# Optimization experiments

Measured on AMD Instinct MI355X. Metric: run time of the kernel, lower is better.

## Reference

```python
import jax, jax.numpy as jnp
import numpy as np

ALPHABET = 26

def _shift(position, S):
    if position == 0:
        return jnp.zeros(S, dtype=jnp.int32)
    elif position == 1:
        return jnp.arange(S, dtype=jnp.int32) % ALPHABET
    elif position == 2:
        return jnp.arange(S, dtype=jnp.int32) // 26 + 1 % 26  # faithful to torch precedence: +1
    elif position == 3:
        return jnp.arange(S, dtype=jnp.int32) // 676 + 1 % 26
    raise ValueError('Invalid rotor position')


def setup_inputs() -> dict:
    key = jax.random.key(0)
    k1, k2 = jax.random.split(key)
    B, S = 128, 8192
    signalInput = jax.random.normal(k1, (B, S, ALPHABET), dtype=jnp.float32)
    # xavier_normal_ on a 26x26 matrix: std = sqrt(2/(26+26))
    std = float(np.sqrt(2.0 / (ALPHABET + ALPHABET)))
    rotor = jax.random.normal(k2, (ALPHABET, ALPHABET), dtype=jnp.float32) * std
    return {"signalInput": signalInput, "rotor": rotor}


def reference(signalInput, rotor):
    position = 1
    B, S, _ = signalInput.shape
    # L2-normalize rotor rows (torch.norm(dim=1, keepdim=True))
    rn = rotor / jnp.linalg.norm(rotor, axis=1, keepdims=True)  # [26,26]
    shift = _shift(position, S)                                  # [S]
    # one_hot((i + shift[s]) % 26) @ rn  ==  gather rn rows
    idx = (jnp.arange(ALPHABET, dtype=jnp.int32)[None, :] + shift[:, None]) % ALPHABET  # [S,26]
    M = rn[idx]                                                  # [S,26,26]
    # per-token 1x26 @ 26x26 bmm, batch-independent rotation matrix
    out = jnp.einsum('bsi,sij->bsj', signalInput, M)             # [B,S,26]
    return jax.nn.softmax(out, axis=2)
```

## Files before the change

### kernel.cpp

```cpp
#include <hip/hip_runtime.h>
#include <math.h>

#define ALPHA 26
#define TPB 256
#define ROWF 26
#define WAVEF (64 * ROWF)

typedef __attribute__((ext_vector_type(8))) short short8;
typedef __attribute__((ext_vector_type(4))) float float4v;
typedef __attribute__((address_space(3))) float lds_f;
typedef const __attribute__((address_space(1))) float glb_f;

__device__ __forceinline__ unsigned short f2bf(float f) {
    unsigned u = __builtin_bit_cast(unsigned, f);
    u += 0x7FFFu + ((u >> 16) & 1u);
    return (unsigned short)(u >> 16);
}

__global__ void rotor_norm_kernel(const float* __restrict__ rotor,
                                  unsigned short* __restrict__ rnb) {
    int k = threadIdx.x;
    if (k < 32) {
        if (k < ALPHA) {
            float ss = 0.f;
            #pragma unroll
            for (int j = 0; j < ALPHA; ++j) {
                float v = rotor[k * ALPHA + j];
                ss += v * v;
            }
            float inv = 1.0f / sqrtf(ss);
            #pragma unroll
            for (int n = 0; n < 32; ++n)
                rnb[k * 32 + n] = (n < ALPHA) ? f2bf(rotor[k * ALPHA + n] * inv)
                                              : (unsigned short)0;
        } else {
            #pragma unroll
            for (int n = 0; n < 32; ++n) rnb[k * 32 + n] = 0;
        }
    }
}

__global__ __launch_bounds__(TPB, 6) void rotor_main(
        const float* __restrict__ x,
        const unsigned short* __restrict__ rnb,
        float* __restrict__ out) {
    __shared__ float stage[4 * WAVEF];

    const int tid  = threadIdx.x;
    const int lane = tid & 63;
    const int wave = tid >> 6;
    const int n15  = lane & 15;
    const int quad = lane >> 4;
    const int waveF = wave * WAVEF;

    short8 bfrag0, bfrag1;
    #pragma unroll
    for (int j = 0; j < 8; ++j) {
        int k = quad * 8 + j;
        bfrag0[j] = (short)rnb[k * 32 + n15];
        bfrag1[j] = (short)rnb[k * 32 + 16 + n15];
    }

    const long long blockF = (long long)blockIdx.x * (TPB * ALPHA);
    const float* gin  = x   + blockF;
    float*       gout = out + blockF;

    #pragma unroll
    for (int it = 0; it < 6; ++it) {
        __builtin_amdgcn_global_load_lds(
            (glb_f*)(gin + waveF + it * 256 + lane * 4),
            (lds_f*)&stage[waveF + it * 256],
            16, 0, 0);
    }
    {
        float2 d = *(const float2*)(gin + waveF + 1536 + lane * 2);
        *(float2*)&stage[waveF + 1536 + lane * 2] = d;
    }
    asm volatile("s_waitcnt vmcnt(0)" ::: "memory");

    const int tokBase = blockIdx.x * TPB + wave * 64;
    float4v accA[4], accB[4];
    #pragma unroll
    for (int m = 0; m < 4; ++m) {
        accA[m] = (float4v){0.f, 0.f, 0.f, 0.f};
        accB[m] = (float4v){0.f, 0.f, 0.f, 0.f};
    }

    #pragma unroll
    for (int m = 0; m < 4; ++m) {
        const int tok = tokBase + m * 16 + n15;
        const int r = (tok & 8191) % 26;
        const int rowOff = waveF + (m * 16 + n15) * ROWF;
        const int k0 = quad * 8;
        int idx0 = k0 - r; if (idx0 < 0) idx0 += 26;

        short8 af;
        #pragma unroll
        for (int j = 0; j < 8; ++j) {
            int idx = idx0 + j; if (idx >= 26) idx -= 26;
            float v = stage[rowOff + idx];
            v = (k0 + j < ALPHA) ? v : 0.f;
            af[j] = (short)f2bf(v);
        }
        accA[m] = __builtin_amdgcn_mfma_f32_16x16x32_bf16(af, bfrag0, accA[m], 0, 0, 0);
        accB[m] = __builtin_amdgcn_mfma_f32_16x16x32_bf16(af, bfrag1, accB[m], 0, 0, 0);
    }

    #pragma unroll
    for (int m = 0; m < 4; ++m) {
        #pragma unroll
        for (int rg = 0; rg < 4; ++rg) {
            const int base = waveF + (m * 16 + quad * 4 + rg) * ROWF;
            stage[base + n15] = accA[m][rg];
            if (n15 < ALPHA - 16)
                stage[base + 16 + n15] = accB[m][rg];
        }
    }
    asm volatile("s_waitcnt lgkmcnt(0)" ::: "memory");

    const float* myrow = &stage[waveF + lane * ROWF];
    float v[ALPHA];
    #pragma unroll
    for (int j = 0; j < ALPHA; ++j) v[j] = myrow[j];
    float mx = v[0];
    #pragma unroll
    for (int j = 1; j < ALPHA; ++j) mx = fmaxf(mx, v[j]);
    float sum = 0.f;
    #pragma unroll
    for (int j = 0; j < ALPHA; ++j) { v[j] = __expf(v[j] - mx); sum += v[j]; }
    float inv = 1.0f / sum;
    float* wrow = &stage[waveF + lane * ROWF];
    #pragma unroll
    for (int j = 0; j < ALPHA; ++j) wrow[j] = v[j] * inv;

    #pragma unroll
    for (int it = 0; it < 6; ++it) {
        float4 d = *(const float4*)&stage[waveF + it * 256 + lane * 4];
        *(float4*)(gout + waveF + it * 256 + lane * 4) = d;
    }
    {
        float2 d = *(const float2*)&stage[waveF + 1536 + lane * 2];
        *(float2*)(gout + waveF + 1536 + lane * 2) = d;
    }
}

extern "C" void kernel_launch(void* const* d_in, const int* in_sizes, int n_in,
                              void* d_out, int out_size, void* d_ws, size_t ws_size,
                              hipStream_t stream) {
    const float* x     = (const float*)d_in[0];
    const float* rotor = (const float*)d_in[1];
    float* out = (float*)d_out;
    unsigned short* rnb = (unsigned short*)d_ws;

    rotor_norm_kernel<<<1, 64, 0, stream>>>(rotor, rnb);

    const int tokens = out_size / ALPHA;
    const int blocks = tokens / TPB;
    rotor_main<<<blocks, TPB, 0, stream>>>(x, rnb, out);
}
```

Before: 193.6 us.

## Make rotor kernel persistent with double-buffered LDS prefetch of next tile

Turns the one-tile-per-block main kernel into a persistent grid-stride loop over at most 768 blocks. Each block double-buffers LDS and issues async global-to-LDS loads for the next tile while computing the current one, so load latency overlaps with MFMA, softmax and stores. The rotor matrix is also stored transposed so each B fragment is a single vector load, and the tail copy now goes through global_load_lds too. In exchange, LDS use per block doubles and launch bounds drop to 3 blocks per CU, which lowers occupancy. Correctness also depends on the hand-written vmcnt count matching the number of loads in flight.

```diff
diff --git a/kernel.cpp b/kernel.cpp
--- a/kernel.cpp
+++ b/kernel.cpp
@@ -5,6 +5,8 @@
 #define TPB 256
 #define ROWF 26
 #define WAVEF (64 * ROWF)
+#define BUFF (4 * WAVEF)
+#define NBLK 768
 
 typedef __attribute__((ext_vector_type(8))) short short8;
 typedef __attribute__((ext_vector_type(4))) float float4v;
@@ -18,33 +20,39 @@
 }
 
 __global__ void rotor_norm_kernel(const float* __restrict__ rotor,
-                                  unsigned short* __restrict__ rnb) {
-    int k = threadIdx.x;
-    if (k < 32) {
-        if (k < ALPHA) {
-            float ss = 0.f;
+                                  unsigned short* __restrict__ rnbT) {
+    __shared__ float inv[32];
+    const int t = threadIdx.x;
+    if (t < 32) {
+        float s = 0.f;
+        if (t < ALPHA) {
             #pragma unroll
             for (int j = 0; j < ALPHA; ++j) {
-                float v = rotor[k * ALPHA + j];
-                ss += v * v;
+                float v = rotor[t * ALPHA + j];
+                s += v * v;
             }
-            float inv = 1.0f / sqrtf(ss);
-            #pragma unroll
-            for (int n = 0; n < 32; ++n)
-                rnb[k * 32 + n] = (n < ALPHA) ? f2bf(rotor[k * ALPHA + n] * inv)
-                                              : (unsigned short)0;
+            inv[t] = 1.0f / sqrtf(s);
         } else {
-            #pragma unroll
-            for (int n = 0; n < 32; ++n) rnb[k * 32 + n] = 0;
+            inv[t] = 0.f;
         }
+    }
+    __syncthreads();
+    const int n  = t >> 1;
+    const int k0 = (t & 1) * 16;
+    #pragma unroll
+    for (int kk = 0; kk < 16; ++kk) {
+        const int k = k0 + kk;
+        float v = (k < ALPHA && n < ALPHA) ? rotor[k * ALPHA + n] * inv[k] : 0.f;
+        rnbT[n * 32 + k] = f2bf(v);
     }
 }
 
-__global__ __launch_bounds__(TPB, 6) void rotor_main(
+__global__ __launch_bounds__(TPB, 3) void rotor_main(
         const float* __restrict__ x,
-        const unsigned short* __restrict__ rnb,
-        float* __restrict__ out) {
-    __shared__ float stage[4 * WAVEF];
+        const unsigned short* __restrict__ rnbT,
+        float* __restrict__ out,
+        int ntiles) {
+    __shared__ float stage[2 * BUFF];
 
     const int tid  = threadIdx.x;
     const int lane = tid & 63;
@@ -53,94 +61,100 @@
     const int quad = lane >> 4;
     const int waveF = wave * WAVEF;
 
-    short8 bfrag0, bfrag1;
-    #pragma unroll
-    for (int j = 0; j < 8; ++j) {
-        int k = quad * 8 + j;
-        bfrag0[j] = (short)rnb[k * 32 + n15];
-        bfrag1[j] = (short)rnb[k * 32 + 16 + n15];
-    }
+    short8 bf0 = *(const short8*)(rnbT + n15 * 32 + quad * 8);
+    short8 bf1 = *(const short8*)(rnbT + (n15 + 16) * 32 + quad * 8);
 
-    const long long blockF = (long long)blockIdx.x * (TPB * ALPHA);
-    const float* gin  = x   + blockF;
-    float*       gout = out + blockF;
+    int tile = blockIdx.x;
+    if (tile >= ntiles) return;
+    const int stride = gridDim.x;
 
-    #pragma unroll
-    for (int it = 0; it < 6; ++it) {
-        __builtin_amdgcn_global_load_lds(
-            (glb_f*)(gin + waveF + it * 256 + lane * 4),
-            (lds_f*)&stage[waveF + it * 256],
-            16, 0, 0);
-    }
-    {
-        float2 d = *(const float2*)(gin + waveF + 1536 + lane * 2);
-        *(float2*)&stage[waveF + 1536 + lane * 2] = d;
-    }
-    asm volatile("s_waitcnt vmcnt(0)" ::: "memory");
+    auto prefetch = [&](int buf, int t) {
+        const float* gp = x + (long long)t * (TPB * ALPHA) + waveF;
+        lds_f* lp = (lds_f*)&stage[buf * BUFF + waveF];
+        #pragma unroll
+        for (int it = 0; it < 6; ++it)
+            __builtin_amdgcn_global_load_lds((glb_f*)(gp + it * 256 + lane * 4),
+                                             lp + it * 256, 16, 0, 0);
+        __builtin_amdgcn_global_load_lds((glb_f*)(gp + 1536 + lane), lp + 1536, 4, 0, 0);
+        __builtin_amdgcn_global_load_lds((glb_f*)(gp + 1600 + lane), lp + 1600, 4, 0, 0);
+    };
 
-    const int tokBase = blockIdx.x * TPB + wave * 64;
-    float4v accA[4], accB[4];
-    #pragma unroll
-    for (int m = 0; m < 4; ++m) {
-        accA[m] = (float4v){0.f, 0.f, 0.f, 0.f};
-        accB[m] = (float4v){0.f, 0.f, 0.f, 0.f};
-    }
+    prefetch(0, tile);
 
-    #pragma unroll
-    for (int m = 0; m < 4; ++m) {
-        const int tok = tokBase + m * 16 + n15;
-        const int r = (tok & 8191) % 26;
-        const int rowOff = waveF + (m * 16 + n15) * ROWF;
-        const int k0 = quad * 8;
-        int idx0 = k0 - r; if (idx0 < 0) idx0 += 26;
+    int i = 0;
+    for (; tile < ntiles; tile += stride, ++i) {
+        if (i == 0) asm volatile("s_waitcnt vmcnt(0)" ::: "memory");
+        else        asm volatile("s_waitcnt vmcnt(7)" ::: "memory");
 
-        short8 af;
+        const int cur = i & 1;
+        const int tnext = tile + stride;
+        if (tnext < ntiles) prefetch(cur ^ 1, tnext);
+        asm volatile("" ::: "memory");
+
+        const int sbase   = cur * BUFF + waveF;
+        const int tokBase = tile * TPB + wave * 64;
+
+        float4v accA[4], accB[4];
         #pragma unroll
-        for (int j = 0; j < 8; ++j) {
-            int idx = idx0 + j; if (idx >= 26) idx -= 26;
-            float v = stage[rowOff + idx];
-            v = (k0 + j < ALPHA) ? v : 0.f;
-            af[j] = (short)f2bf(v);
+        for (int m = 0; m < 4; ++m) {
+            accA[m] = (float4v){0.f, 0.f, 0.f, 0.f};
+            accB[m] = (float4v){0.f, 0.f, 0.f, 0.f};
         }
-        accA[m] = __builtin_amdgcn_mfma_f32_16x16x32_bf16(af, bfrag0, accA[m], 0, 0, 0);
-        accB[m] = __builtin_amdgcn_mfma_f32_16x16x32_bf16(af, bfrag1, accB[m], 0, 0, 0);
-    }
 
-    #pragma unroll
-    for (int m = 0; m < 4; ++m) {
         #pragma unroll
-        for (int rg = 0; rg < 4; ++rg) {
-            const int base = waveF + (m * 16 + quad * 4 + rg) * ROWF;
-            stage[base + n15] = accA[m][rg];
-            if (n15 < ALPHA - 16)
-                stage[base + 16 + n15] = accB[m][rg];
+        for (int m = 0; m < 4; ++m) {
+            const int tok = tokBase + m * 16 + n15;
+            const int r = (tok & 8191) % 26;
+            const int rowOff = sbase + (m * 16 + n15) * ROWF;
+            const int k0 = quad * 8;
+            int idx0 = k0 - r; if (idx0 < 0) idx0 += 26;
+
+            short8 af;
+            #pragma unroll
+            for (int j = 0; j < 8; ++j) {
+                int idx = idx0 + j; if (idx >= 26) idx -= 26;
+                af[j] = (short)f2bf(stage[rowOff + idx]);
+            }
+            accA[m] = __builtin_amdgcn_mfma_f32_16x16x32_bf16(af, bf0, accA[m], 0, 0, 0);
+            accB[m] = __builtin_amdgcn_mfma_f32_16x16x32_bf16(af, bf1, accB[m], 0, 0, 0);
         }
-    }
-    asm volatile("s_waitcnt lgkmcnt(0)" ::: "memory");
 
-    const float* myrow = &stage[waveF + lane * ROWF];
-    float v[ALPHA];
-    #pragma unroll
-    for (int j = 0; j < ALPHA; ++j) v[j] = myrow[j];
-    float mx = v[0];
-    #pragma unroll
-    for (int j = 1; j < ALPHA; ++j) mx = fmaxf(mx, v[j]);
-    float sum = 0.f;
-    #pragma unroll
-    for (int j = 0; j < ALPHA; ++j) { v[j] = __expf(v[j] - mx); sum += v[j]; }
-    float inv = 1.0f / sum;
-    float* wrow = &stage[waveF + lane * ROWF];
-    #pragma unroll
-    for (int j = 0; j < ALPHA; ++j) wrow[j] = v[j] * inv;
+        #pragma unroll
+        for (int m = 0; m < 4; ++m) {
+            #pragma unroll
+            for (int rg = 0; rg < 4; ++rg) {
+                const int base = sbase + (m * 16 + quad * 4 + rg) * ROWF;
+                stage[base + n15] = accA[m][rg];
+                if (n15 < ALPHA - 16)
+                    stage[base + 16 + n15] = accB[m][rg];
+            }
+        }
 
-    #pragma unroll
-    for (int it = 0; it < 6; ++it) {
-        float4 d = *(const float4*)&stage[waveF + it * 256 + lane * 4];
-        *(float4*)(gout + waveF + it * 256 + lane * 4) = d;
-    }
-    {
-        float2 d = *(const float2*)&stage[waveF + 1536 + lane * 2];
-        *(float2*)(gout + waveF + 1536 + lane * 2) = d;
+        const float* myrow = &stage[sbase + lane * ROWF];
+        float v[ALPHA];
+        #pragma unroll
+        for (int j = 0; j < ALPHA; ++j) v[j] = myrow[j];
+        float mx = v[0];
+        #pragma unroll
+        for (int j = 1; j < ALPHA; ++j) mx = fmaxf(mx, v[j]);
+        float sum = 0.f;
+        #pragma unroll
+        for (int j = 0; j < ALPHA; ++j) { v[j] = __expf(v[j] - mx); sum += v[j]; }
+        float inv = 1.0f / sum;
+        float* wrow = &stage[sbase + lane * ROWF];
+        #pragma unroll
+        for (int j = 0; j < ALPHA; ++j) wrow[j] = v[j] * inv;
+
+        float* gout = out + (long long)tile * (TPB * ALPHA) + waveF;
+        #pragma unroll
+        for (int it = 0; it < 6; ++it) {
+            float4 d = *(const float4*)&stage[sbase + it * 256 + lane * 4];
+            *(float4*)(gout + it * 256 + lane * 4) = d;
+        }
+        {
+            float2 d = *(const float2*)&stage[sbase + 1536 + lane * 2];
+            *(float2*)(gout + 1536 + lane * 2) = d;
+        }
     }
 }
 
@@ -150,11 +164,12 @@
     const float* x     = (const float*)d_in[0];
     const float* rotor = (const float*)d_in[1];
     float* out = (float*)d_out;
-    unsigned short* rnb = (unsigned short*)d_ws;
+    unsigned short* rnbT = (unsigned short*)d_ws;
 
-    rotor_norm_kernel<<<1, 64, 0, stream>>>(rotor, rnb);
+    rotor_norm_kernel<<<1, 64, 0, stream>>>(rotor, rnbT);
 
     const int tokens = out_size / ALPHA;
-    const int blocks = tokens / TPB;
-    rotor_main<<<blocks, TPB, 0, stream>>>(x, rnb, out);
+    const int tiles  = tokens / TPB;
+    const int grid   = (tiles < NBLK) ? tiles : NBLK;
+    rotor_main<<<grid, TPB, 0, stream>>>(x, rnbT, out, tiles);
 }
```

After: 198.1 us. +2.3%, slower.
